# Kernel optimization log

Hardware: AMD Instinct MI355X
Metric: run time of the kernel (lower is better)

## Reference

```python
import jax, jax.numpy as jnp
import numpy as np

B, T, L, V, E, H = 128, 64, 2, 32000, 768, 768
G = 4 * H  # gate dim
EPS = 1e-5


def setup_inputs() -> dict:
    key = jax.random.key(0)
    ks = jax.random.split(key, 12)
    s = 1.0 / np.sqrt(H)
    message = jax.random.randint(ks[0], (B, T), 0, V, dtype=jnp.int64)
    message_lengths = jax.random.randint(ks[1], (B,), 1, T + 1, dtype=jnp.int64)
    return {
        "message": message,
        "message_lengths": message_lengths,
        "embedding_table": jax.random.normal(ks[2], (V, E), jnp.float32),
        "W_ih": jax.random.uniform(ks[3], (L, G, E), jnp.float32, -s, s),
        "W_hh": jax.random.uniform(ks[4], (L, G, H), jnp.float32, -s, s),
        "b_ih": jax.random.uniform(ks[5], (L, G), jnp.float32, -s, s),
        "b_hh": jax.random.uniform(ks[6], (L, G), jnp.float32, -s, s),
        "gamma_h": 1.0 + 0.1 * jax.random.normal(ks[7], (H,), jnp.float32),
        "beta_h": 0.1 * jax.random.normal(ks[8], (H,), jnp.float32),
        "gamma_c": 1.0 + 0.1 * jax.random.normal(ks[9], (H,), jnp.float32),
        "beta_c": 0.1 * jax.random.normal(ks[10], (H,), jnp.float32),
    }


def _layernorm(x, g, b):
    mu = jnp.mean(x, axis=-1, keepdims=True)
    var = jnp.mean(jnp.square(x - mu), axis=-1, keepdims=True)
    return (x - mu) * jax.lax.rsqrt(var + EPS) * g + b


def reference(message, message_lengths, embedding_table, W_ih, W_hh, b_ih, b_hh,
              gamma_h, beta_h, gamma_c, beta_c):
    emb = embedding_table[message]  # [B, T, E]
    # Precompute input projections for all steps/layers (every layer sees the
    # raw embedding at each step, matching the original code).
    x_proj = jnp.einsum('bte,lge->tblg', emb, W_ih) + b_ih  # [T, B, L, G]
    mask = jnp.ones((B, H), emb.dtype)  # dropout_rate=None -> ones mask

    h0 = jnp.zeros((L, B, H), emb.dtype)
    c0 = jnp.zeros((L, B, H), emb.dtype)

    def step(carry, x_t):  # x_t: [B, L, G]
        h, c = carry
        new_h, new_c = [], []
        h_last = None
        for l in range(L):
            gates = x_t[:, l] + h[l] @ W_hh[l].T + b_hh[l]  # [B, G]
            i_g, f_g, g_g, o_g = jnp.split(gates, 4, axis=-1)
            c_t = jax.nn.sigmoid(f_g) * c[l] + jax.nn.sigmoid(i_g) * jnp.tanh(g_g)
            h_t = jax.nn.sigmoid(o_g) * jnp.tanh(c_t)
            h_t = _layernorm(h_t * mask, gamma_h, beta_h)
            c_t = _layernorm(c_t, gamma_c, beta_c)
            new_h.append(h_t)
            new_c.append(c_t)
            h_last = h_t
        return (jnp.stack(new_h), jnp.stack(new_c)), h_last

    _, hidden_all = jax.lax.scan(step, (h0, c0), x_proj)  # [T, B, H]
    hidden_all = hidden_all.transpose(1, 0, 2)  # [B, T, H]
    idx = (message_lengths - 1)[:, None, None]  # [B, 1, 1]
    encoded = jnp.take_along_axis(hidden_all, idx, axis=1)[:, 0]  # [B, H]
    return encoded
```

## Files before the change

kernel.cpp:

```cpp
#include <hip/hip_runtime.h>
#include <stdint.h>

#define T_LEN 64
#define B_SZ  128
#define H_SZ  768
#define G_SZ  3072
#define E_SZ  768
#define LN_EPS 1e-5f

typedef __bf16 bf16x8 __attribute__((ext_vector_type(8)));
typedef float  f32x4  __attribute__((ext_vector_type(4)));
typedef short  short8 __attribute__((ext_vector_type(8)));

__device__ __forceinline__ float bf2f(unsigned short h) {
  unsigned int u = ((unsigned int)h) << 16;
  return __builtin_bit_cast(float, u);
}
__device__ __forceinline__ unsigned short f2bf(float f) {
  unsigned int u = __builtin_bit_cast(unsigned int, f);
  u += 0x7fffu + ((u >> 16) & 1u);
  return (unsigned short)(u >> 16);
}
__device__ __forceinline__ void split8(float4 v0, float4 v1, short8& hi, short8& lo) {
  float v[8] = {v0.x, v0.y, v0.z, v0.w, v1.x, v1.y, v1.z, v1.w};
#pragma unroll
  for (int j = 0; j < 8; ++j) {
    unsigned short h = f2bf(v[j]);
    hi[j] = (short)h;
    lo[j] = (short)f2bf(v[j] - bf2f(h));
  }
}
__device__ __forceinline__ void st_wt(void* p, unsigned long long v) {
  __hip_atomic_store((unsigned long long*)p, v, __ATOMIC_RELAXED,
                     __HIP_MEMORY_SCOPE_AGENT);
}

__global__ void prep_kernel(const int* __restrict__ msg,
                            const float* __restrict__ table,
                            const float* __restrict__ W_ih,
                            const float* __restrict__ W_hh,
                            const float* __restrict__ b_ih,
                            const float* __restrict__ b_hh,
                            const float* __restrict__ gamma_h,
                            const float* __restrict__ beta_h,
                            unsigned short* __restrict__ A_hi,
                            unsigned short* __restrict__ A_lo,
                            unsigned short* __restrict__ Wih_hi,
                            unsigned short* __restrict__ Wih_lo,
                            unsigned short* __restrict__ Whh_hi,
                            unsigned short* __restrict__ Whh_lo,
                            float* __restrict__ SWp,
                            float* __restrict__ Sbeta,
                            float* __restrict__ bias,
                            unsigned int* __restrict__ bar) {
  int idx = blockIdx.x * blockDim.x + threadIdx.x;
  int stride = gridDim.x * blockDim.x;
  for (int c = idx; c < 8192 * 96; c += stride) {
    int n = c / 96;
    int ko = (c - n * 96) * 8;
    int b = n & 127, t = n >> 7;
    int m = msg[b * T_LEN + t];
    const float4* s4 = (const float4*)(table + (size_t)m * E_SZ + ko);
    short8 hi, lo;
    split8(s4[0], s4[1], hi, lo);
    *(short8*)(A_hi + (size_t)n * E_SZ + ko) = hi;
    *(short8*)(A_lo + (size_t)n * E_SZ + ko) = lo;
  }
  for (int c = idx; c < G_SZ * E_SZ / 8; c += stride) {
    int o8 = c * 8;
    {
      const float4* s4 = (const float4*)(W_ih + (size_t)G_SZ * E_SZ + o8);
      short8 hi, lo;
      split8(s4[0], s4[1], hi, lo);
      *(short8*)(Wih_hi + o8) = hi;
      *(short8*)(Wih_lo + o8) = lo;
    }
    {
      int g = o8 / H_SZ;
      int j = o8 - g * H_SZ;
      const float4* s4 = (const float4*)(W_hh + (size_t)G_SZ * H_SZ + o8);
      const float4* g4 = (const float4*)(gamma_h + j);
      float4 v0 = s4[0], v1 = s4[1];
      float4 w0 = g4[0], w1 = g4[1];
      v0.x *= w0.x; v0.y *= w0.y; v0.z *= w0.z; v0.w *= w0.w;
      v1.x *= w1.x; v1.y *= w1.y; v1.z *= w1.z; v1.w *= w1.w;
      short8 hi, lo;
      split8(v0, v1, hi, lo);
      *(short8*)(Whh_hi + o8) = hi;
      *(short8*)(Whh_lo + o8) = lo;
    }
  }
  for (int g = idx; g < G_SZ; g += stride) {
    const float4* wr = (const float4*)(W_hh + (size_t)G_SZ * H_SZ + (size_t)g * H_SZ);
    const float4* gm = (const float4*)gamma_h;
    const float4* bt = (const float4*)beta_h;
    float sw = 0.f, sb = 0.f;
    for (int i = 0; i < H_SZ / 4; ++i) {
      float4 wv = wr[i], gv = gm[i], bv = bt[i];
      sw += wv.x * gv.x + wv.y * gv.y + wv.z * gv.z + wv.w * gv.w;
      sb += wv.x * bv.x + wv.y * bv.y + wv.z * bv.z + wv.w * bv.w;
    }
    SWp[g] = sw;
    Sbeta[g] = sb;
    bias[g] = b_ih[G_SZ + g] + b_hh[G_SZ + g];
  }
  for (int c = idx; c < 18432; c += stride) bar[c] = 0u;
}

#define K2_STR 56

__global__ __launch_bounds__(256) void xproj_kernel(
    const unsigned short* __restrict__ A_hi, const unsigned short* __restrict__ A_lo,
    const unsigned short* __restrict__ B_hi, const unsigned short* __restrict__ B_lo,
    const float* __restrict__ bias, void* __restrict__ Xout, int x_is_f32) {
  __shared__ float smemf[7168];
  unsigned short* AsH = (unsigned short*)smemf;
  unsigned short* AsL = AsH + 64 * K2_STR;
  unsigned short* BsH = AsL + 64 * K2_STR;
  unsigned short* BsL = BsH + 64 * K2_STR;

  int bid = blockIdx.x;
  int mchunk = bid / 384;
  int r = bid - mchunk * 384;
  int nb = r >> 3;
  int mb = (mchunk << 3) + (r & 7);
  int m0 = mb * 64, n0 = nb * 64;
  int tid = threadIdx.x;
  int w = tid >> 6, lane = tid & 63;
  int wm = w & 1, wn = w >> 1;
  int rs = tid >> 2, ks = (tid & 3) * 8;
  int lrow = lane & 15, lk = (lane >> 4) * 8;

  f32x4 acc[2][2] = {};
  const unsigned short* gA = A_hi + (size_t)(m0 + rs) * E_SZ + ks;
  const unsigned short* gAl = A_lo + (size_t)(m0 + rs) * E_SZ + ks;
  const unsigned short* gB = B_hi + (size_t)(n0 + rs) * E_SZ + ks;
  const unsigned short* gBl = B_lo + (size_t)(n0 + rs) * E_SZ + ks;
  short8 vah = *(const short8*)gA;
  short8 val = *(const short8*)gAl;
  short8 vbh = *(const short8*)gB;
  short8 vbl = *(const short8*)gBl;
  for (int kt = 0; kt < 24; ++kt) {
    __syncthreads();
    *(short8*)(AsH + rs * K2_STR + ks) = vah;
    *(short8*)(AsL + rs * K2_STR + ks) = val;
    *(short8*)(BsH + rs * K2_STR + ks) = vbh;
    *(short8*)(BsL + rs * K2_STR + ks) = vbl;
    __syncthreads();
    if (kt < 23) {
      int k0 = (kt + 1) * 32;
      vah = *(const short8*)(gA + k0);
      val = *(const short8*)(gAl + k0);
      vbh = *(const short8*)(gB + k0);
      vbl = *(const short8*)(gBl + k0);
    }
    bf16x8 ah0 = *(const bf16x8*)(AsH + (wm * 32 +      lrow) * K2_STR + lk);
    bf16x8 ah1 = *(const bf16x8*)(AsH + (wm * 32 + 16 + lrow) * K2_STR + lk);
    bf16x8 al0 = *(const bf16x8*)(AsL + (wm * 32 +      lrow) * K2_STR + lk);
    bf16x8 al1 = *(const bf16x8*)(AsL + (wm * 32 + 16 + lrow) * K2_STR + lk);
    bf16x8 bh0 = *(const bf16x8*)(BsH + (wn * 32 +      lrow) * K2_STR + lk);
    bf16x8 bh1 = *(const bf16x8*)(BsH + (wn * 32 + 16 + lrow) * K2_STR + lk);
    bf16x8 bl0 = *(const bf16x8*)(BsL + (wn * 32 +      lrow) * K2_STR + lk);
    bf16x8 bl1 = *(const bf16x8*)(BsL + (wn * 32 + 16 + lrow) * K2_STR + lk);
    acc[0][0] = __builtin_amdgcn_mfma_f32_16x16x32_bf16(ah0, bh0, acc[0][0], 0, 0, 0);
    acc[1][0] = __builtin_amdgcn_mfma_f32_16x16x32_bf16(ah1, bh0, acc[1][0], 0, 0, 0);
    acc[0][1] = __builtin_amdgcn_mfma_f32_16x16x32_bf16(ah0, bh1, acc[0][1], 0, 0, 0);
    acc[1][1] = __builtin_amdgcn_mfma_f32_16x16x32_bf16(ah1, bh1, acc[1][1], 0, 0, 0);
    acc[0][0] = __builtin_amdgcn_mfma_f32_16x16x32_bf16(al0, bh0, acc[0][0], 0, 0, 0);
    acc[1][0] = __builtin_amdgcn_mfma_f32_16x16x32_bf16(al1, bh0, acc[1][0], 0, 0, 0);
    acc[0][1] = __builtin_amdgcn_mfma_f32_16x16x32_bf16(al0, bh1, acc[0][1], 0, 0, 0);
    acc[1][1] = __builtin_amdgcn_mfma_f32_16x16x32_bf16(al1, bh1, acc[1][1], 0, 0, 0);
    acc[0][0] = __builtin_amdgcn_mfma_f32_16x16x32_bf16(ah0, bl0, acc[0][0], 0, 0, 0);
    acc[1][0] = __builtin_amdgcn_mfma_f32_16x16x32_bf16(ah1, bl0, acc[1][0], 0, 0, 0);
    acc[0][1] = __builtin_amdgcn_mfma_f32_16x16x32_bf16(ah0, bl1, acc[0][1], 0, 0, 0);
    acc[1][1] = __builtin_amdgcn_mfma_f32_16x16x32_bf16(ah1, bl1, acc[1][1], 0, 0, 0);
  }
  __syncthreads();
  float* Cs = smemf;
  int quad = lane >> 4;
#pragma unroll
  for (int mt = 0; mt < 2; ++mt)
#pragma unroll
    for (int nt = 0; nt < 2; ++nt) {
      int mloc = wm * 32 + mt * 16 + quad * 4;
      int nloc = wn * 32 + nt * 16 + lrow;
#pragma unroll
      for (int rr = 0; rr < 4; ++rr) Cs[nloc * 72 + mloc + rr] = acc[mt][nt][rr];
    }
  __syncthreads();
  int t = mb >> 1, bbase = (mb & 1) * 64;
#pragma unroll
  for (int rep = 0; rep < 2; ++rep) {
    int n = (tid >> 3) + rep * 32;
    int c = (tid & 7) * 8;
    float bv = bias[n0 + n];
    float v[8];
#pragma unroll
    for (int j = 0; j < 8; ++j) v[j] = Cs[n * 72 + c + j] + bv;
    size_t off = ((size_t)t * G_SZ + (n0 + n)) * B_SZ + bbase + c;
    if (x_is_f32) {
      float4* dst = (float4*)((float*)Xout + off);
      dst[0] = make_float4(v[0], v[1], v[2], v[3]);
      dst[1] = make_float4(v[4], v[5], v[6], v[7]);
    } else {
      short8 o;
#pragma unroll
      for (int j = 0; j < 8; ++j) o[j] = (short)f2bf(v[j]);
      *(short8*)((unsigned short*)Xout + off) = o;
    }
  }
}

__device__ __forceinline__ void gridbar(unsigned int* leaf, unsigned int* root,
                                        int idx, int sub) {
  __syncthreads();
  if (threadIdx.x == 0) {
    asm volatile("" ::: "memory");
    unsigned int old = __hip_atomic_fetch_add(&leaf[idx * 128 + sub * 16], 1u,
                                              __ATOMIC_RELAXED, __HIP_MEMORY_SCOPE_AGENT);
    if (old == 11u)
      __hip_atomic_fetch_add(&root[idx * 16], 1u,
                             __ATOMIC_RELAXED, __HIP_MEMORY_SCOPE_AGENT);
    while (__hip_atomic_load(&root[idx * 16], __ATOMIC_RELAXED,
                             __HIP_MEMORY_SCOPE_AGENT) < 8u)
      __builtin_amdgcn_s_sleep(2);
    asm volatile("" ::: "memory");
  }
  __syncthreads();
}

extern __shared__ char lstm_smem[];

__global__ __launch_bounds__(128) void lstm_kernel(
    const unsigned short* __restrict__ Whh_lo,
    const unsigned short* __restrict__ Whh_hi,
    const void* __restrict__ X, int x_is_f32,
    const float* __restrict__ SWp, const float* __restrict__ Sbeta,
    const float* __restrict__ gamma_h, const float* __restrict__ beta_h,
    const float* __restrict__ gamma_c, const float* __restrict__ beta_c,
    const int* __restrict__ lens,
    unsigned short* __restrict__ Hbuf, float* __restrict__ part,
    unsigned int* __restrict__ bar, float* __restrict__ out) {
  unsigned short* WtH = (unsigned short*)lstm_smem;
  unsigned short* WtL = WtH + 32 * 776;
  float* glds   = (float*)(WtL + 32 * 776);
  float* pstat2 = glds + 2304;
  float* rstat4 = pstat2 + 512;
  float* rstat  = rstat4 + 256;
  float* ghs = rstat + 256;
  float* bhs = ghs + 8;
  float* gcs = bhs + 8;
  float* bcs = gcs + 8;

  int bidx = blockIdx.x;
  int jb = bidx % 96, rb = bidx / 96;
  int j0 = jb * 8, b0 = rb * 64;
  int tid = threadIdx.x;
  int w = tid >> 6, lane = tid & 63;
  int lrow = lane & 15, lkq = lane >> 4;
  int sub = jb / 12;
  unsigned int* leaf = bar;
  unsigned int* root = bar + 16384;

  for (int c = tid; c < 3072; c += 128) {
    int row = c / 96, ko = (c - row * 96) * 8;
    size_t goff = ((size_t)((row >> 3) * H_SZ + j0 + (row & 7))) * H_SZ + ko;
    *(short8*)(&WtH[row * 776 + ko]) = *(const short8*)(Whh_hi + goff);
    *(short8*)(&WtL[row * 776 + ko]) = *(const short8*)(Whh_lo + goff);
  }
  if (tid < 8) {
    ghs[tid] = gamma_h[j0 + tid]; bhs[tid] = beta_h[j0 + tid];
    gcs[tid] = gamma_c[j0 + tid]; bcs[tid] = beta_c[j0 + tid];
  }

  int row = tid & 63;
  int half = tid >> 6;
  int jjq = half * 4;
  int mylen = lens[b0 + row];
  int myWrow = (w << 4) | lrow;
  int gate4 = myWrow >> 3, jjl = myWrow & 7;
  int g_global = gate4 * H_SZ + j0 + jjl;
  float mySW = SWp[g_global];
  float mySb = Sbeta[g_global];
  const unsigned short* wbase = &WtH[(size_t)myWrow * 776];
  const unsigned short* wlob  = &WtL[(size_t)myWrow * 776];
  float c4[4], h4[4];
  float xv[4][4];
  __syncthreads();

  {
    size_t xbase = ((size_t)0 * G_SZ + g_global) * B_SZ + b0 + lkq * 4;
#pragma unroll
    for (int mt = 0; mt < 4; ++mt) {
      float xr[4];
      if (x_is_f32) {
        float4 p = *(const float4*)((const float*)X + xbase + mt * 16);
        xr[0] = p.x; xr[1] = p.y; xr[2] = p.z; xr[3] = p.w;
      } else {
        ushort4 p = *(const ushort4*)((const unsigned short*)X + xbase + mt * 16);
        xr[0] = bf2f(p.x); xr[1] = bf2f(p.y); xr[2] = bf2f(p.z); xr[3] = bf2f(p.w);
      }
#pragma unroll
      for (int rr = 0; rr < 4; ++rr)
        glds[(gate4 * 8 + jjl) * 72 + mt * 16 + lkq * 4 + rr] = xr[rr];
    }
  }
  __syncthreads();
  {
    float ph = 0.f, ph2 = 0.f, pc = 0.f, pc2 = 0.f;
#pragma unroll
    for (int q = 0; q < 4; ++q) {
      int jj = jjq + q;
      float iv = glds[(0 * 8 + jj) * 72 + row];
      float gv = glds[(2 * 8 + jj) * 72 + row];
      float ov = glds[(3 * 8 + jj) * 72 + row];
      float si = 1.f / (1.f + expf(-iv));
      float so = 1.f / (1.f + expf(-ov));
      float cn = si * tanhf(gv);
      float hp = so * tanhf(cn);
      c4[q] = cn; h4[q] = hp;
      ph += hp; ph2 += hp * hp; pc += cn; pc2 += cn * cn;
    }
    size_t hx = (((size_t)0 * 128 + b0 + row) * 96 + jb) * 16 + jjq;
    ushort4 hiv, lov;
    hiv.x = f2bf(h4[0]); hiv.y = f2bf(h4[1]); hiv.z = f2bf(h4[2]); hiv.w = f2bf(h4[3]);
    lov.x = f2bf(h4[0] - bf2f(hiv.x)); lov.y = f2bf(h4[1] - bf2f(hiv.y));
    lov.z = f2bf(h4[2] - bf2f(hiv.z)); lov.w = f2bf(h4[3] - bf2f(hiv.w));
    st_wt(&Hbuf[hx], __builtin_bit_cast(unsigned long long, hiv));
    st_wt(&Hbuf[hx + 8], __builtin_bit_cast(unsigned long long, lov));
    *(f32x4*)&pstat2[(row * 2 + half) * 4] = f32x4{ph, ph2, pc, pc2};
  }
  __syncthreads();
  {
    int f = tid * 2;
    float2 v;
    v.x = pstat2[(f >> 2) * 8 + (f & 3)] + pstat2[(f >> 2) * 8 + 4 + (f & 3)];
    v.y = pstat2[((f + 1) >> 2) * 8 + ((f + 1) & 3)] +
          pstat2[((f + 1) >> 2) * 8 + 4 + ((f + 1) & 3)];
    st_wt(&part[((size_t)(0 * 2 + rb) * 96 + jb) * 256 + f],
          __builtin_bit_cast(unsigned long long, v));
  }
  {
    size_t xbase = ((size_t)1 * G_SZ + g_global) * B_SZ + b0 + lkq * 4;
#pragma unroll
    for (int mt = 0; mt < 4; ++mt) {
      if (x_is_f32) {
        float4 p = *(const float4*)((const float*)X + xbase + mt * 16);
        xv[mt][0] = p.x; xv[mt][1] = p.y; xv[mt][2] = p.z; xv[mt][3] = p.w;
      } else {
        ushort4 p = *(const ushort4*)((const unsigned short*)X + xbase + mt * 16);
        xv[mt][0] = bf2f(p.x); xv[mt][1] = bf2f(p.y);
        xv[mt][2] = bf2f(p.z); xv[mt][3] = bf2f(p.w);
      }
    }
  }
  gridbar(leaf, root, 0 * 2 + rb, sub);

  for (int t = 1; t < T_LEN; ++t) {
    f32x4 acc[4] = {};
    {
      const unsigned short* hb[4];
#pragma unroll
      for (int mt = 0; mt < 4; ++mt)
        hb[mt] = Hbuf + ((size_t)(t - 1) * 128 + b0 + mt * 16 + lrow) * 1536;
#pragma unroll 4
      for (int kt = 0; kt < 24; ++kt) {
        int k0 = kt * 32 + lkq * 8;
        int co = (kt * 4 + lkq) * 16;
        bf16x8 wh = *(const bf16x8*)(wbase + k0);
        bf16x8 wl = *(const bf16x8*)(wlob + k0);
#pragma unroll
        for (int mt = 0; mt < 4; ++mt) {
          bf16x8 ah = *(const bf16x8*)(hb[mt] + co);
          bf16x8 al = *(const bf16x8*)(hb[mt] + co + 8);
          acc[mt] = __builtin_amdgcn_mfma_f32_16x16x32_bf16(ah, wh, acc[mt], 0, 0, 0);
          acc[mt] = __builtin_amdgcn_mfma_f32_16x16x32_bf16(al, wh, acc[mt], 0, 0, 0);
          acc[mt] = __builtin_amdgcn_mfma_f32_16x16x32_bf16(ah, wl, acc[mt], 0, 0, 0);
        }
      }
    }
    float psum0 = 0.f, psum1 = 0.f;
    {
      const float* pb = part + ((size_t)((t - 1) * 2 + rb) * 96) * 256 + tid * 2;
#pragma unroll 24
      for (int j = 0; j < 96; ++j) {
        float2 v = *(const float2*)(pb + j * 256);
        psum0 += v.x; psum1 += v.y;
      }
    }
    {
      int f = tid * 2;
      rstat4[f] = psum0;
      rstat4[f + 1] = psum1;
    }
    __syncthreads();
    if (tid < 64) {
      f32x4 s = *(f32x4*)&rstat4[tid * 4];
      float muh = s[0] * (1.f / 768.f), muc = s[2] * (1.f / 768.f);
      float vh = s[1] * (1.f / 768.f) - muh * muh;
      float vc = s[3] * (1.f / 768.f) - muc * muc;
      float rh = rsqrtf(vh + LN_EPS), rc = rsqrtf(vc + LN_EPS);
      *(f32x4*)&rstat[tid * 4] = f32x4{rh, muh * rh, rc, muc * rc};
    }
    __syncthreads();
    if (mylen == t) {
      float2 rv = *(float2*)&rstat[row * 4];
#pragma unroll
      for (int q = 0; q < 4; ++q)
        out[(size_t)(b0 + row) * H_SZ + j0 + jjq + q] =
            (rv.x * h4[q] - rv.y) * ghs[jjq + q] + bhs[jjq + q];
    }
#pragma unroll
    for (int mt = 0; mt < 4; ++mt) {
#pragma unroll
      for (int rr = 0; rr < 4; ++rr) {
        int r2 = mt * 16 + lkq * 4 + rr;
        float2 rv = *(float2*)&rstat[r2 * 4];
        glds[(gate4 * 8 + jjl) * 72 + r2] =
            xv[mt][rr] + rv.x * acc[mt][rr] - rv.y * mySW + mySb;
      }
    }
    __syncthreads();
    {
      f32x4 rv = *(f32x4*)&rstat[row * 4];
      float ph = 0.f, ph2 = 0.f, pc = 0.f, pc2 = 0.f;
#pragma unroll
      for (int q = 0; q < 4; ++q) {
        int jj = jjq + q;
        float cprev = (rv[2] * c4[q] - rv[3]) * gcs[jj] + bcs[jj];
        float iv = glds[(0 * 8 + jj) * 72 + row];
        float fv = glds[(1 * 8 + jj) * 72 + row];
        float gv = glds[(2 * 8 + jj) * 72 + row];
        float ov = glds[(3 * 8 + jj) * 72 + row];
        float si = 1.f / (1.f + expf(-iv));
        float sf = 1.f / (1.f + expf(-fv));
        float so = 1.f / (1.f + expf(-ov));
        float cn = sf * cprev + si * tanhf(gv);
        float hp = so * tanhf(cn);
        c4[q] = cn; h4[q] = hp;
        ph += hp; ph2 += hp * hp; pc += cn; pc2 += cn * cn;
      }
      size_t hx = (((size_t)t * 128 + b0 + row) * 96 + jb) * 16 + jjq;
      ushort4 hiv, lov;
      hiv.x = f2bf(h4[0]); hiv.y = f2bf(h4[1]); hiv.z = f2bf(h4[2]); hiv.w = f2bf(h4[3]);
      lov.x = f2bf(h4[0] - bf2f(hiv.x)); lov.y = f2bf(h4[1] - bf2f(hiv.y));
      lov.z = f2bf(h4[2] - bf2f(hiv.z)); lov.w = f2bf(h4[3] - bf2f(hiv.w));
      st_wt(&Hbuf[hx], __builtin_bit_cast(unsigned long long, hiv));
      st_wt(&Hbuf[hx + 8], __builtin_bit_cast(unsigned long long, lov));
      *(f32x4*)&pstat2[(row * 2 + half) * 4] = f32x4{ph, ph2, pc, pc2};
    }
    __syncthreads();
    {
      int f = tid * 2;
      float2 v;
      v.x = pstat2[(f >> 2) * 8 + (f & 3)] + pstat2[(f >> 2) * 8 + 4 + (f & 3)];
      v.y = pstat2[((f + 1) >> 2) * 8 + ((f + 1) & 3)] +
            pstat2[((f + 1) >> 2) * 8 + 4 + ((f + 1) & 3)];
      st_wt(&part[((size_t)(t * 2 + rb) * 96 + jb) * 256 + f],
            __builtin_bit_cast(unsigned long long, v));
    }
    if (t < T_LEN - 1) {
      size_t xbase = ((size_t)(t + 1) * G_SZ + g_global) * B_SZ + b0 + lkq * 4;
#pragma unroll
      for (int mt = 0; mt < 4; ++mt) {
        if (x_is_f32) {
          float4 p = *(const float4*)((const float*)X + xbase + mt * 16);
          xv[mt][0] = p.x; xv[mt][1] = p.y; xv[mt][2] = p.z; xv[mt][3] = p.w;
        } else {
          ushort4 p = *(const ushort4*)((const unsigned short*)X + xbase + mt * 16);
          xv[mt][0] = bf2f(p.x); xv[mt][1] = bf2f(p.y);
          xv[mt][2] = bf2f(p.z); xv[mt][3] = bf2f(p.w);
        }
      }
    }
    gridbar(leaf, root, t * 2 + rb, sub);
  }

  {
    float psum0 = 0.f, psum1 = 0.f;
    const float* pb = part + ((size_t)(63 * 2 + rb) * 96) * 256 + tid * 2;
#pragma unroll 24
    for (int j = 0; j < 96; ++j) {
      float2 v = *(const float2*)(pb + j * 256);
      psum0 += v.x; psum1 += v.y;
    }
    rstat4[tid * 2] = psum0;
    rstat4[tid * 2 + 1] = psum1;
  }
  __syncthreads();
  if (tid < 64) {
    f32x4 s = *(f32x4*)&rstat4[tid * 4];
    float muh = s[0] * (1.f / 768.f);
    float vh = s[1] * (1.f / 768.f) - muh * muh;
    float rh = rsqrtf(vh + LN_EPS);
    rstat[tid * 4] = rh;
    rstat[tid * 4 + 1] = muh * rh;
  }
  __syncthreads();
  if (mylen == T_LEN) {
    float2 rv = *(float2*)&rstat[row * 4];
#pragma unroll
    for (int q = 0; q < 4; ++q)
      out[(size_t)(b0 + row) * H_SZ + j0 + jjq + q] =
          (rv.x * h4[q] - rv.y) * ghs[jjq + q] + bhs[jjq + q];
  }
}

#define LSTM_LDS_BYTES 112896

extern "C" void kernel_launch(void* const* d_in, const int* in_sizes, int n_in,
                              void* d_out, int out_size, void* d_ws, size_t ws_size,
                              hipStream_t stream) {
  const int*   msg     = (const int*)d_in[0];
  const int*   lens    = (const int*)d_in[1];
  const float* table   = (const float*)d_in[2];
  const float* W_ih    = (const float*)d_in[3];
  const float* W_hh    = (const float*)d_in[4];
  const float* b_ih    = (const float*)d_in[5];
  const float* b_hh    = (const float*)d_in[6];
  const float* gamma_h = (const float*)d_in[7];
  const float* beta_h  = (const float*)d_in[8];
  const float* gamma_c = (const float*)d_in[9];
  const float* beta_c  = (const float*)d_in[10];
  float* out = (float*)d_out;

  static int attr_done = 0;
  if (!attr_done) {
    hipFuncSetAttribute((const void*)lstm_kernel,
                        hipFuncAttributeMaxDynamicSharedMemorySize,
                        LSTM_LDS_BYTES);
    attr_done = 1;
  }

  size_t szA = (size_t)8192 * 768 * 2;
  size_t szW = (size_t)3072 * 768 * 2;
  size_t szF = 3072 * 4;
  size_t szH = (size_t)T_LEN * 128 * 96 * 16 * 2;
  size_t szBar = 18432 * 4;
  size_t rest = 2 * szA + 4 * szW + 3 * szF + szH + szBar;
  size_t xf32 = (size_t)64 * 3072 * 128 * 4;
  int x_is_f32 = (ws_size >= xf32 + rest) ? 1 : 0;

  char* p = (char*)d_ws;
  void* X = (void*)p;               p += x_is_f32 ? xf32 : (xf32 / 2);
  unsigned short* A_hi   = (unsigned short*)p; p += szA;
  unsigned short* A_lo   = (unsigned short*)p; p += szA;
  unsigned short* Wih_hi = (unsigned short*)p; p += szW;
  unsigned short* Wih_lo = (unsigned short*)p; p += szW;
  unsigned short* Whh_hi = (unsigned short*)p; p += szW;
  unsigned short* Whh_lo = (unsigned short*)p; p += szW;
  float* SWp   = (float*)p;         p += szF;
  float* Sbeta = (float*)p;         p += szF;
  float* bias  = (float*)p;         p += szF;
  unsigned short* Hbuf = (unsigned short*)p; p += szH;
  unsigned int* bar = (unsigned int*)p;      p += szBar;
  float* part = (float*)A_hi;

  hipLaunchKernelGGL(prep_kernel, dim3(1024), dim3(256), 0, stream,
                     msg, table, W_ih, W_hh, b_ih, b_hh, gamma_h, beta_h,
                     A_hi, A_lo, Wih_hi, Wih_lo, Whh_hi, Whh_lo,
                     SWp, Sbeta, bias, bar);
  hipLaunchKernelGGL(xproj_kernel, dim3(6144), dim3(256), 0, stream,
                     A_hi, A_lo, Wih_hi, Wih_lo, bias, X, x_is_f32);

  void* kargs[] = { (void*)&Whh_lo, (void*)&Whh_hi, (void*)&X, (void*)&x_is_f32,
                    (void*)&SWp, (void*)&Sbeta,
                    (void*)&gamma_h, (void*)&beta_h, (void*)&gamma_c, (void*)&beta_c,
                    (void*)&lens, (void*)&Hbuf, (void*)&part,
                    (void*)&bar, (void*)&out };
  hipLaunchCooperativeKernel((void*)lstm_kernel, dim3(192), dim3(128), kargs,
                             LSTM_LDS_BYTES, stream);
}
```

Measured before the change: 1.779 ms.

## Add stats-reduction warps to overlap LayerNorm partial sums with MFMA, release-flag grid barrier

Each LSTM block grows from 128 to 256 threads. The extra two waves reduce the cross-block LayerNorm partial sums, reading float4 per thread, while the first two waves run the recurrent MFMA, so the global reduction runs alongside the matmul instead of after it. The grid barrier also changes: the last arriver writes per-subgroup release flags, and waiters poll their own flag rather than all spinning on one root counter. This costs more registers and threads per block, plus a larger barrier workspace that must be zeroed.

```diff
diff --git a/kernel.cpp b/kernel.cpp
--- a/kernel.cpp
+++ b/kernel.cpp
@@ -33,6 +33,9 @@
 __device__ __forceinline__ void st_wt(void* p, unsigned long long v) {
   __hip_atomic_store((unsigned long long*)p, v, __ATOMIC_RELAXED,
                      __HIP_MEMORY_SCOPE_AGENT);
+}
+__device__ __forceinline__ void st_wt32(unsigned int* p, unsigned int v) {
+  __hip_atomic_store(p, v, __ATOMIC_RELAXED, __HIP_MEMORY_SCOPE_AGENT);
 }
 
 __global__ void prep_kernel(const int* __restrict__ msg,
@@ -104,7 +107,7 @@
     Sbeta[g] = sb;
     bias[g] = b_ih[G_SZ + g] + b_hh[G_SZ + g];
   }
-  for (int c = idx; c < 18432; c += stride) bar[c] = 0u;
+  for (int c = idx; c < 34816; c += stride) bar[c] = 0u;
 }
 
 #define K2_STR 56
@@ -212,18 +215,27 @@
 }
 
 __device__ __forceinline__ void gridbar(unsigned int* leaf, unsigned int* root,
-                                        int idx, int sub) {
+                                        unsigned int* rel, int idx, int sub) {
   __syncthreads();
   if (threadIdx.x == 0) {
     asm volatile("" ::: "memory");
+    bool released = false;
     unsigned int old = __hip_atomic_fetch_add(&leaf[idx * 128 + sub * 16], 1u,
                                               __ATOMIC_RELAXED, __HIP_MEMORY_SCOPE_AGENT);
-    if (old == 11u)
-      __hip_atomic_fetch_add(&root[idx * 16], 1u,
-                             __ATOMIC_RELAXED, __HIP_MEMORY_SCOPE_AGENT);
-    while (__hip_atomic_load(&root[idx * 16], __ATOMIC_RELAXED,
-                             __HIP_MEMORY_SCOPE_AGENT) < 8u)
-      __builtin_amdgcn_s_sleep(2);
+    if (old == 11u) {
+      unsigned int rold = __hip_atomic_fetch_add(&root[idx * 16], 1u,
+                                                 __ATOMIC_RELAXED, __HIP_MEMORY_SCOPE_AGENT);
+      if (rold == 7u) {
+#pragma unroll
+        for (int s = 0; s < 8; ++s) st_wt32(&rel[idx * 128 + s * 16], 1u);
+        released = true;
+      }
+    }
+    if (!released) {
+      while (__hip_atomic_load(&rel[idx * 128 + sub * 16], __ATOMIC_RELAXED,
+                               __HIP_MEMORY_SCOPE_AGENT) == 0u)
+        __builtin_amdgcn_s_sleep(1);
+    }
     asm volatile("" ::: "memory");
   }
   __syncthreads();
@@ -231,7 +243,7 @@
 
 extern __shared__ char lstm_smem[];
 
-__global__ __launch_bounds__(128) void lstm_kernel(
+__global__ __launch_bounds__(256) void lstm_kernel(
     const unsigned short* __restrict__ Whh_lo,
     const unsigned short* __restrict__ Whh_hi,
     const void* __restrict__ X, int x_is_f32,
@@ -261,8 +273,9 @@
   int sub = jb / 12;
   unsigned int* leaf = bar;
   unsigned int* root = bar + 16384;
-
-  for (int c = tid; c < 3072; c += 128) {
+  unsigned int* rel  = bar + 18432;
+
+  for (int c = tid; c < 3072; c += 256) {
     int row = c / 96, ko = (c - row * 96) * 8;
     size_t goff = ((size_t)((row >> 3) * H_SZ + j0 + (row & 7))) * H_SZ + ko;
     *(short8*)(&WtH[row * 776 + ko]) = *(const short8*)(Whh_hi + goff);
@@ -274,10 +287,10 @@
   }
 
   int row = tid & 63;
-  int half = tid >> 6;
+  int half = (tid >> 6) & 1;
   int jjq = half * 4;
   int mylen = lens[b0 + row];
-  int myWrow = (w << 4) | lrow;
+  int myWrow = ((w & 1) << 4) | lrow;
   int gate4 = myWrow >> 3, jjl = myWrow & 7;
   int g_global = gate4 * H_SZ + j0 + jjl;
   float mySW = SWp[g_global];
@@ -286,9 +299,10 @@
   const unsigned short* wlob  = &WtL[(size_t)myWrow * 776];
   float c4[4], h4[4];
   float xv[4][4];
-  __syncthreads();
-
-  {
+  int stid = tid - 128;
+  __syncthreads();
+
+  if (tid < 128) {
     size_t xbase = ((size_t)0 * G_SZ + g_global) * B_SZ + b0 + lkq * 4;
 #pragma unroll
     for (int mt = 0; mt < 4; ++mt) {
@@ -306,7 +320,7 @@
     }
   }
   __syncthreads();
-  {
+  if (tid < 128) {
     float ph = 0.f, ph2 = 0.f, pc = 0.f, pc2 = 0.f;
 #pragma unroll
     for (int q = 0; q < 4; ++q) {
@@ -331,7 +345,7 @@
     *(f32x4*)&pstat2[(row * 2 + half) * 4] = f32x4{ph, ph2, pc, pc2};
   }
   __syncthreads();
-  {
+  if (tid < 128) {
     int f = tid * 2;
     float2 v;
     v.x = pstat2[(f >> 2) * 8 + (f & 3)] + pstat2[(f >> 2) * 8 + 4 + (f & 3)];
@@ -339,8 +353,6 @@
           pstat2[((f + 1) >> 2) * 8 + 4 + ((f + 1) & 3)];
     st_wt(&part[((size_t)(0 * 2 + rb) * 96 + jb) * 256 + f],
           __builtin_bit_cast(unsigned long long, v));
-  }
-  {
     size_t xbase = ((size_t)1 * G_SZ + g_global) * B_SZ + b0 + lkq * 4;
 #pragma unroll
     for (int mt = 0; mt < 4; ++mt) {
@@ -354,11 +366,11 @@
       }
     }
   }
-  gridbar(leaf, root, 0 * 2 + rb, sub);
+  gridbar(leaf, root, rel, 0 * 2 + rb, sub);
 
   for (int t = 1; t < T_LEN; ++t) {
     f32x4 acc[4] = {};
-    {
+    if (tid < 128) {
       const unsigned short* hb[4];
 #pragma unroll
       for (int mt = 0; mt < 4; ++mt)
@@ -378,50 +390,42 @@
           acc[mt] = __builtin_amdgcn_mfma_f32_16x16x32_bf16(ah, wl, acc[mt], 0, 0, 0);
         }
       }
-    }
-    float psum0 = 0.f, psum1 = 0.f;
-    {
-      const float* pb = part + ((size_t)((t - 1) * 2 + rb) * 96) * 256 + tid * 2;
+    } else if (stid < 64) {
+      const float* pb = part + ((size_t)((t - 1) * 2 + rb) * 96) * 256 + stid * 4;
+      f32x4 s = {};
 #pragma unroll 24
       for (int j = 0; j < 96; ++j) {
-        float2 v = *(const float2*)(pb + j * 256);
-        psum0 += v.x; psum1 += v.y;
-      }
-    }
-    {
-      int f = tid * 2;
-      rstat4[f] = psum0;
-      rstat4[f + 1] = psum1;
-    }
-    __syncthreads();
-    if (tid < 64) {
-      f32x4 s = *(f32x4*)&rstat4[tid * 4];
+        f32x4 v = *(const f32x4*)(pb + j * 256);
+        s[0] += v[0]; s[1] += v[1]; s[2] += v[2]; s[3] += v[3];
+      }
       float muh = s[0] * (1.f / 768.f), muc = s[2] * (1.f / 768.f);
       float vh = s[1] * (1.f / 768.f) - muh * muh;
       float vc = s[3] * (1.f / 768.f) - muc * muc;
       float rh = rsqrtf(vh + LN_EPS), rc = rsqrtf(vc + LN_EPS);
-      *(f32x4*)&rstat[tid * 4] = f32x4{rh, muh * rh, rc, muc * rc};
+      *(f32x4*)&rstat[stid * 4] = f32x4{rh, muh * rh, rc, muc * rc};
     }
     __syncthreads();
-    if (mylen == t) {
-      float2 rv = *(float2*)&rstat[row * 4];
-#pragma unroll
-      for (int q = 0; q < 4; ++q)
-        out[(size_t)(b0 + row) * H_SZ + j0 + jjq + q] =
-            (rv.x * h4[q] - rv.y) * ghs[jjq + q] + bhs[jjq + q];
-    }
-#pragma unroll
-    for (int mt = 0; mt < 4; ++mt) {
-#pragma unroll
-      for (int rr = 0; rr < 4; ++rr) {
-        int r2 = mt * 16 + lkq * 4 + rr;
-        float2 rv = *(float2*)&rstat[r2 * 4];
-        glds[(gate4 * 8 + jjl) * 72 + r2] =
-            xv[mt][rr] + rv.x * acc[mt][rr] - rv.y * mySW + mySb;
+    if (tid < 128) {
+      if (mylen == t) {
+        float2 rv = *(float2*)&rstat[row * 4];
+#pragma unroll
+        for (int q = 0; q < 4; ++q)
+          out[(size_t)(b0 + row) * H_SZ + j0 + jjq + q] =
+              (rv.x * h4[q] - rv.y) * ghs[jjq + q] + bhs[jjq + q];
+      }
+#pragma unroll
+      for (int mt = 0; mt < 4; ++mt) {
+#pragma unroll
+        for (int rr = 0; rr < 4; ++rr) {
+          int r2 = mt * 16 + lkq * 4 + rr;
+          float2 rv = *(float2*)&rstat[r2 * 4];
+          glds[(gate4 * 8 + jjl) * 72 + r2] =
+              xv[mt][rr] + rv.x * acc[mt][rr] - rv.y * mySW + mySb;
+        }
       }
     }
     __syncthreads();
-    {
+    if (tid < 128) {
       f32x4 rv = *(f32x4*)&rstat[row * 4];
       float ph = 0.f, ph2 = 0.f, pc = 0.f, pc2 = 0.f;
 #pragma unroll
@@ -450,7 +454,7 @@
       *(f32x4*)&pstat2[(row * 2 + half) * 4] = f32x4{ph, ph2, pc, pc2};
     }
     __syncthreads();
-    {
+    if (tid < 128) {
       int f = tid * 2;
       float2 v;
       v.x = pstat2[(f >> 2) * 8 + (f & 3)] + pstat2[(f >> 2) * 8 + 4 + (f & 3)];
@@ -458,46 +462,40 @@
             pstat2[((f + 1) >> 2) * 8 + 4 + ((f + 1) & 3)];
       st_wt(&part[((size_t)(t * 2 + rb) * 96 + jb) * 256 + f],
             __builtin_bit_cast(unsigned long long, v));
-    }
-    if (t < T_LEN - 1) {
-      size_t xbase = ((size_t)(t + 1) * G_SZ + g_global) * B_SZ + b0 + lkq * 4;
-#pragma unroll
-      for (int mt = 0; mt < 4; ++mt) {
-        if (x_is_f32) {
-          float4 p = *(const float4*)((const float*)X + xbase + mt * 16);
-          xv[mt][0] = p.x; xv[mt][1] = p.y; xv[mt][2] = p.z; xv[mt][3] = p.w;
-        } else {
-          ushort4 p = *(const ushort4*)((const unsigned short*)X + xbase + mt * 16);
-          xv[mt][0] = bf2f(p.x); xv[mt][1] = bf2f(p.y);
-          xv[mt][2] = bf2f(p.z); xv[mt][3] = bf2f(p.w);
+      if (t < T_LEN - 1) {
+        size_t xbase = ((size_t)(t + 1) * G_SZ + g_global) * B_SZ + b0 + lkq * 4;
+#pragma unroll
+        for (int mt = 0; mt < 4; ++mt) {
+          if (x_is_f32) {
+            float4 p = *(const float4*)((const float*)X + xbase + mt * 16);
+            xv[mt][0] = p.x; xv[mt][1] = p.y; xv[mt][2] = p.z; xv[mt][3] = p.w;
+          } else {
+            ushort4 p = *(const ushort4*)((const unsigned short*)X + xbase + mt * 16);
+            xv[mt][0] = bf2f(p.x); xv[mt][1] = bf2f(p.y);
+            xv[mt][2] = bf2f(p.z); xv[mt][3] = bf2f(p.w);
+          }
         }
       }
     }
-    gridbar(leaf, root, t * 2 + rb, sub);
-  }
-
-  {
-    float psum0 = 0.f, psum1 = 0.f;
-    const float* pb = part + ((size_t)(63 * 2 + rb) * 96) * 256 + tid * 2;
+    gridbar(leaf, root, rel, t * 2 + rb, sub);
+  }
+
+  if (tid >= 128 && stid < 64) {
+    const float* pb = part + ((size_t)(63 * 2 + rb) * 96) * 256 + stid * 4;
+    f32x4 s = {};
 #pragma unroll 24
     for (int j = 0; j < 96; ++j) {
-      float2 v = *(const float2*)(pb + j * 256);
-      psum0 += v.x; psum1 += v.y;
-    }
-    rstat4[tid * 2] = psum0;
-    rstat4[tid * 2 + 1] = psum1;
-  }
-  __syncthreads();
-  if (tid < 64) {
-    f32x4 s = *(f32x4*)&rstat4[tid * 4];
+      f32x4 v = *(const f32x4*)(pb + j * 256);
+      s[0] += v[0]; s[1] += v[1]; s[2] += v[2]; s[3] += v[3];
+    }
     float muh = s[0] * (1.f / 768.f);
     float vh = s[1] * (1.f / 768.f) - muh * muh;
     float rh = rsqrtf(vh + LN_EPS);
-    rstat[tid * 4] = rh;
-    rstat[tid * 4 + 1] = muh * rh;
-  }
-  __syncthreads();
-  if (mylen == T_LEN) {
+    rstat[stid * 4] = rh;
+    rstat[stid * 4 + 1] = muh * rh;
+  }
+  __syncthreads();
+  if (tid < 128 && mylen == T_LEN) {
     float2 rv = *(float2*)&rstat[row * 4];
 #pragma unroll
     for (int q = 0; q < 4; ++q)
@@ -536,7 +534,7 @@
   size_t szW = (size_t)3072 * 768 * 2;
   size_t szF = 3072 * 4;
   size_t szH = (size_t)T_LEN * 128 * 96 * 16 * 2;
-  size_t szBar = 18432 * 4;
+  size_t szBar = 34816 * 4;
   size_t rest = 2 * szA + 4 * szW + 3 * szF + szH + szBar;
   size_t xf32 = (size_t)64 * 3072 * 128 * 4;
   int x_is_f32 = (ws_size >= xf32 + rest) ? 1 : 0;
@@ -568,6 +566,6 @@
                     (void*)&gamma_h, (void*)&beta_h, (void*)&gamma_c, (void*)&beta_c,
                     (void*)&lens, (void*)&Hbuf, (void*)&part,
                     (void*)&bar, (void*)&out };
-  hipLaunchCooperativeKernel((void*)lstm_kernel, dim3(192), dim3(128), kargs,
+  hipLaunchCooperativeKernel((void*)lstm_kernel, dim3(192), dim3(256), kargs,
                              LSTM_LDS_BYTES, stream);
 }
```

Result: slower. 2.345 ms (+31.8%).
